# Optimization experiments

Measured on AMD Instinct MI355X. Metric: run time of the kernel, lower is better.

## Reference

```python
import jax, jax.numpy as jnp
import numpy as np
from jax import lax

EPS = 1e-5


def setup_inputs() -> dict:
    key = jax.random.key(0)
    ks = jax.random.split(key, 8)
    b, c_in, h, w = 16, 256, 64, 64
    c_out, kh, n_exp = 512, 3, 8
    fan_in = c_in * kh * kh
    bound_w = float(np.sqrt(6.0 / fan_in))  # kaiming_uniform a=sqrt(5) -> U(-sqrt(6/fan_in), +)
    bound_b = float(1.0 / np.sqrt(fan_in))
    return {
        "x": jax.random.normal(ks[0], (b, c_in, h, w), dtype=jnp.float32),
        "expert_weight": jax.random.uniform(ks[1], (n_exp, c_out, c_in, kh, kh), jnp.float32, -bound_w, bound_w),
        "expert_bias": jax.random.uniform(ks[2], (n_exp, c_out), jnp.float32, -bound_b, bound_b),
        "fc_w": jax.random.uniform(ks[3], (n_exp, c_in), jnp.float32, -1.0 / np.sqrt(c_in), 1.0 / np.sqrt(c_in)),
        "fc_b": jax.random.uniform(ks[4], (n_exp,), jnp.float32, -1.0 / np.sqrt(c_in), 1.0 / np.sqrt(c_in)),
        "bn_gamma": jnp.ones((c_out,), jnp.float32),
        "bn_beta": jnp.zeros((c_out,), jnp.float32),
    }


def reference(x, expert_weight, expert_bias, fc_w, fc_b, bn_gamma, bn_beta):
    # --- route_func: GAP -> Linear -> sigmoid -> (b, k) ---
    pooled = x.mean(axis=(2, 3))                       # (b, c_in)
    routing = jax.nn.sigmoid(pooled @ fc_w.T + fc_b)   # (b, k)

    # --- per-sample combined kernels and biases ---
    comb_w = jnp.einsum('bk,koihw->boihw', routing, expert_weight)  # (b, c_out, c_in, kh, kw)
    comb_b = routing @ expert_bias                                  # (b, c_out)

    # --- per-sample conv (equivalent of groups=b grouped conv) ---
    def conv_one(xi, wi):
        # xi: (c_in, h, w), wi: (c_out, c_in, kh, kw)
        return lax.conv_general_dilated(
            xi[None], wi, window_strides=(1, 1), padding=[(1, 1), (1, 1)],
            rhs_dilation=(1, 1), dimension_numbers=('NCHW', 'OIHW', 'NCHW'))[0]

    out = jax.vmap(conv_one)(x, comb_w) + comb_b[:, :, None, None]  # (b, c_out, h, w)

    # --- BatchNorm2d (training mode: batch statistics) ---
    mean = out.mean(axis=(0, 2, 3))
    var = out.var(axis=(0, 2, 3))
    out = (out - mean[None, :, None, None]) * (bn_gamma * lax.rsqrt(var + EPS))[None, :, None, None] \
          + bn_beta[None, :, None, None]

    # --- LeakyReLU(0.1) ---
    return jnp.where(out > 0, out, 0.1 * out)
```

## Files before the change

kernel.cpp:

```cpp
#include <hip/hip_runtime.h>
#include <hip/hip_bf16.h>
#include <stdint.h>

typedef unsigned short u16;
typedef short bf16x8 __attribute__((ext_vector_type(8)));
typedef float f32x4 __attribute__((ext_vector_type(4)));
typedef u16 u16x8 __attribute__((ext_vector_type(8)));

#define DEVFN static __device__ __forceinline__

#define NB 16
#define CIN 256
#define HH 64
#define WW 64
#define COUT 512
#define NPX 4096
#define NSTEP 72

DEVFN u16 bf16_rne(float f){
  union { float f; uint32_t u; } v; v.f = f;
  uint32_t u = v.u;
  return (u16)((u + 0x7fffu + ((u >> 16) & 1u)) >> 16);
}

DEVFN void gload16(const void* g, void* l){
  __builtin_amdgcn_global_load_lds((const __attribute__((address_space(1))) void*)g,
                                   (__attribute__((address_space(3))) void*)l,
                                   16, 0, 0);
}

#define VMWAIT(N) asm volatile("s_waitcnt vmcnt(" #N ")" ::: "memory")
#define LGKM0() do { asm volatile("s_waitcnt lgkmcnt(0)" ::: "memory"); \
                     __builtin_amdgcn_sched_barrier(0); } while(0)
#define BARRIER() do { __builtin_amdgcn_s_barrier(); \
                       __builtin_amdgcn_sched_barrier(0); \
                       asm volatile("" ::: "memory"); } while(0)

__global__ void k_route(const float* __restrict__ pooled, const float* __restrict__ fcw,
                        const float* __restrict__ fcb, float* __restrict__ routing){
  int bk = blockIdx.x;
  int b = bk >> 3, k = bk & 7;
  int l = threadIdx.x;
  float4 pv = ((const float4*)(pooled + b*CIN))[l];
  float4 wv = ((const float4*)(fcw   + k*CIN))[l];
  float s = pv.x*wv.x + pv.y*wv.y + pv.z*wv.z + pv.w*wv.w;
  for (int o = 32; o; o >>= 1) s += __shfl_down(s, o);
  if (l == 0) routing[b*8 + k] = 1.0f / (1.0f + __expf(-(s * (1.0f/(float)NPX) + fcb[k])));
}

__global__ void k_cbias(const float* __restrict__ routing, const float* __restrict__ eb,
                        float* __restrict__ cbias){
  int idx = blockIdx.x*256 + threadIdx.x;
  int b = idx >> 9, co = idx & 511;
  float s = 0.f;
  for (int k = 0; k < 8; k++) s += routing[b*8+k] * eb[k*COUT + co];
  cbias[idx] = s;
}

__global__ void k_wcomb(const float* __restrict__ routing, const float* __restrict__ ew,
                        u16* __restrict__ wc){
  int blk  = blockIdx.x;
  int step = blk >> 6;
  int cog  = blk & 63;
  int cb = step / 9, rs = step - cb*9;
  int t = threadIdx.x;
  int ci = t & 31, co = cog*8 + (t >> 5);
  int cig = cb*32 + ci;
  float wv[8];
#pragma unroll
  for (int k = 0; k < 8; k++)
    wv[k] = ew[(size_t)((k*COUT + co)*CIN + cig)*9 + rs];
  for (int b = 0; b < NB; b++){
    float s = 0.f;
#pragma unroll
    for (int k = 0; k < 8; k++) s += routing[b*8+k] * wv[k];
    wc[((size_t)(b*NSTEP + step)*COUT + co)*32 + ci] = bf16_rne(s);
  }
}

__global__ void k_halo(u16* __restrict__ xt){
  int blk = blockIdx.x;
  int b = blk / 66, row = blk - b*66;
  uint32_t* base = (uint32_t*)(xt + ((size_t)(b*66 + row))*68*256);
  int t = threadIdx.x;
  if (row == 0 || row == 65){
    for (int i = t; i < 8704; i += 256) base[i] = 0;
  } else {
    for (int i = t; i < 512; i += 256){
      int idx = (i < 128) ? i : (8320 + (i - 128));
      base[idx] = 0;
    }
  }
}

__global__ void k_xprep(const float* __restrict__ x, u16* __restrict__ xt,
                        float* __restrict__ pooled){
  int blk = blockIdx.x;
  int ctile = blk & 3;
  int h = (blk >> 2) & 63;
  int b = blk >> 8;
  __shared__ u16 S[64][66];
  int t = threadIdx.x;
  {
    int ci_l = t >> 2, w0 = (t & 3) * 16;
    const float4* src = (const float4*)(x + ((size_t)((b*CIN + ctile*64 + ci_l)*HH + h)*WW + w0));
    float4 a = src[0], bb = src[1], c = src[2], d = src[3];
    u16* row = &S[ci_l][w0];
    row[0]=bf16_rne(a.x);  row[1]=bf16_rne(a.y);  row[2]=bf16_rne(a.z);  row[3]=bf16_rne(a.w);
    row[4]=bf16_rne(bb.x); row[5]=bf16_rne(bb.y); row[6]=bf16_rne(bb.z); row[7]=bf16_rne(bb.w);
    row[8]=bf16_rne(c.x);  row[9]=bf16_rne(c.y);  row[10]=bf16_rne(c.z); row[11]=bf16_rne(c.w);
    row[12]=bf16_rne(d.x); row[13]=bf16_rne(d.y); row[14]=bf16_rne(d.z); row[15]=bf16_rne(d.w);
    float s = a.x+a.y+a.z+a.w + bb.x+bb.y+bb.z+bb.w + c.x+c.y+c.z+c.w + d.x+d.y+d.z+d.w;
    s += __shfl_down(s, 2);
    s += __shfl_down(s, 1);
    if ((t & 3) == 0) atomicAdd(&pooled[b*CIN + ctile*64 + ci_l], s);
  }
  __syncthreads();
  {
    int w_l = t >> 2, cig = (t & 3) * 16;
    u16x8 v0, v1;
#pragma unroll
    for (int j = 0; j < 8; j++){ v0[j] = S[cig+j][w_l]; v1[j] = S[cig+8+j][w_l]; }
    u16* dst = xt + ((size_t)(b*66 + h + 1)*68 + (w_l + 1))*CIN + ctile*64 + cig;
    *(u16x8*)(dst)     = v0;
    *(u16x8*)(dst + 8) = v1;
  }
}

#define WBYTES 16384
#define XBYTES 26112

template<int H>
DEVFN void stage_w_half(const u16* __restrict__ wstep, char* dst, int wv, int l){
  int qb = H*512 + wv*64;
  int q  = qb + l;
  int co_l = q >> 2, j = q & 3;
  gload16(wstep + co_l*32 + ((j ^ ((co_l >> 1) & 3)) << 3), dst + qb*16);
  __builtin_amdgcn_sched_barrier(0);
}

template<int C>
DEVFN void stage_x_chunk(const u16* __restrict__ xtb, int h0, int cioff, char* dst,
                         int wv, int l){
  int qb = C*512 + wv*64;
  if (qb >= 1632) qb -= 1632;
  int q = qb + l;
  int t2 = q >> 2;
  int lr = (t2 * 964) >> 16;
  int c  = t2 - lr*68;
  int j  = q & 3;
  gload16(xtb + ((size_t)(h0 + lr)*68 + c)*CIN + cioff + ((j ^ ((c >> 1) & 3)) << 3),
          dst + qb*16);
  __builtin_amdgcn_sched_barrier(0);
}

template<int RS>
DEVFN void conv_step(int cb, char* ldsW, const char* Xc, char* Xn,
                     const u16* __restrict__ xtb, const u16* __restrict__ wcb, int h0,
                     int wv, int l, int wm, int wn, int l15, int kbq,
                     f32x4 acc[4][8])
{
  constexpr int r = RS/3, s = RS - r*3;
  const char* Wc = ldsW + (RS % 3)*WBYTES;
  char* Wp       = ldsW + ((RS + 2) % 3)*WBYTES;
  const u16* wnext = wcb + (size_t)(cb*9 + RS + 2)*(COUT*32);
  const bool dostage = (RS <= 6) || (cb < 7);

  bf16x8 wf[4], xf[4];
  const int swzA = (kbq ^ ((l15 >> 1) & 3)) << 4;
#pragma unroll
  for (int nf = 0; nf < 4; nf++)
    wf[nf] = *(const bf16x8*)(Wc + (wn*64 + nf*16 + l15)*64 + swzA);
  {
    int row = wm*2 + r;
#pragma unroll
    for (int mf = 0; mf < 4; mf++){
      int c0 = mf*16 + l15 + s;
      xf[mf] = *(const bf16x8*)(Xc + (row*68 + c0)*64 + ((kbq ^ ((c0 >> 1) & 3)) << 4));
    }
  }
  if (dostage) stage_w_half<0>(wnext, Wp, wv, l);
  BARRIER();
  LGKM0();
  __builtin_amdgcn_s_setprio(1);
#pragma unroll
  for (int nf = 0; nf < 4; nf++)
#pragma unroll
    for (int mf = 0; mf < 4; mf++)
      acc[nf][mf] = __builtin_amdgcn_mfma_f32_16x16x32_bf16(wf[nf], xf[mf], acc[nf][mf], 0, 0, 0);
  __builtin_amdgcn_s_setprio(0);
  BARRIER();

  {
    int row = wm*2 + 1 + r;
#pragma unroll
    for (int mf = 0; mf < 4; mf++){
      int c0 = mf*16 + l15 + s;
      xf[mf] = *(const bf16x8*)(Xc + (row*68 + c0)*64 + ((kbq ^ ((c0 >> 1) & 3)) << 4));
    }
  }
  if (dostage) stage_w_half<1>(wnext, Wp, wv, l);
  if constexpr (RS <= 3) { if (cb < 7) stage_x_chunk<RS>(xtb, h0, (cb+1)*32, Xn, wv, l); }
  if (dostage) { VMWAIT(2); }
  else if constexpr (RS == 7) { VMWAIT(0); }
  BARRIER();
  LGKM0();
  __builtin_amdgcn_s_setprio(1);
#pragma unroll
  for (int nf = 0; nf < 4; nf++)
#pragma unroll
    for (int mf = 0; mf < 4; mf++)
      acc[nf][mf+4] = __builtin_amdgcn_mfma_f32_16x16x32_bf16(wf[nf], xf[mf], acc[nf][mf+4], 0, 0, 0);
  __builtin_amdgcn_s_setprio(0);
  BARRIER();
}

__global__ __launch_bounds__(512, 2) void k_conv(
    const u16* __restrict__ xt, const u16* __restrict__ wc,
    const float* __restrict__ cbias, float* __restrict__ out, u16* __restrict__ obf,
    float* __restrict__ ssum, float* __restrict__ ssq)
{
  __shared__ char lds[3*WBYTES + 2*XBYTES];
  char* XA = lds + 3*WBYTES;
  char* XB = lds + 3*WBYTES + XBYTES;

  int hw  = blockIdx.x;
  int xcd = hw & 7;
  int i   = hw >> 3;
  int b   = xcd*2 + (i >> 5);
  int ct  = (i >> 4) & 1;
  int pt  = i & 15;
  int h0  = pt * 4;

  int t = threadIdx.x, l = t & 63, wv = t >> 6;
  int wm = wv >> 2, wn = wv & 3;
  int l15 = l & 15, kbq = l >> 4;

  const u16* xtb = xt + (size_t)b * 66*68*CIN;
  const u16* wcb = wc + (size_t)(b*NSTEP) * COUT*32 + ct*256*32;

  f32x4 acc[4][8];
#pragma unroll
  for (int nf = 0; nf < 4; nf++)
#pragma unroll
    for (int mf = 0; mf < 8; mf++) acc[nf][mf] = (f32x4){0.f,0.f,0.f,0.f};

  stage_x_chunk<0>(xtb, h0, 0, XA, wv, l);
  stage_x_chunk<1>(xtb, h0, 0, XA, wv, l);
  stage_x_chunk<2>(xtb, h0, 0, XA, wv, l);
  stage_x_chunk<3>(xtb, h0, 0, XA, wv, l);
  stage_w_half<0>(wcb,           lds + 0*WBYTES, wv, l);
  stage_w_half<1>(wcb,           lds + 0*WBYTES, wv, l);
  stage_w_half<0>(wcb + COUT*32, lds + 1*WBYTES, wv, l);
  stage_w_half<1>(wcb + COUT*32, lds + 1*WBYTES, wv, l);
  VMWAIT(0);
  BARRIER();

  for (int cb = 0; cb < 8; cb++){
    const char* Xc = (cb & 1) ? XB : XA;
    char*       Xn = (cb & 1) ? XA : XB;
    conv_step<0>(cb, lds, Xc, Xn, xtb, wcb, h0, wv,l,wm,wn,l15,kbq, acc);
    conv_step<1>(cb, lds, Xc, Xn, xtb, wcb, h0, wv,l,wm,wn,l15,kbq, acc);
    conv_step<2>(cb, lds, Xc, Xn, xtb, wcb, h0, wv,l,wm,wn,l15,kbq, acc);
    conv_step<3>(cb, lds, Xc, Xn, xtb, wcb, h0, wv,l,wm,wn,l15,kbq, acc);
    conv_step<4>(cb, lds, Xc, Xn, xtb, wcb, h0, wv,l,wm,wn,l15,kbq, acc);
    conv_step<5>(cb, lds, Xc, Xn, xtb, wcb, h0, wv,l,wm,wn,l15,kbq, acc);
    conv_step<6>(cb, lds, Xc, Xn, xtb, wcb, h0, wv,l,wm,wn,l15,kbq, acc);
    conv_step<7>(cb, lds, Xc, Xn, xtb, wcb, h0, wv,l,wm,wn,l15,kbq, acc);
    conv_step<8>(cb, lds, Xc, Xn, xtb, wcb, h0, wv,l,wm,wn,l15,kbq, acc);
  }

#pragma unroll
  for (int nf = 0; nf < 4; nf++){
#pragma unroll
    for (int rg = 0; rg < 4; rg++){
      int co = ct*256 + wn*64 + nf*16 + (kbq << 2) + rg;
      float bias = cbias[b*COUT + co];
      float s1 = 0.f, s2 = 0.f;
      size_t base = ((size_t)b * COUT + co) * NPX;
#pragma unroll
      for (int mf = 0; mf < 8; mf++){
        float v = acc[nf][mf][rg] + bias;
        int px = (h0 + wm*2 + (mf >> 2))*64 + (mf & 3)*16 + l15;
        if (obf) obf[base + px] = bf16_rne(v);
        else     out[base + px] = v;
        s1 += v; s2 += v*v;
      }
#pragma unroll
      for (int o = 8; o; o >>= 1){ s1 += __shfl_xor(s1, o); s2 += __shfl_xor(s2, o); }
      if (l15 == 0){ atomicAdd(&ssum[co], s1); atomicAdd(&ssq[co], s2); }
    }
  }
}

__global__ void k_stats(const float* __restrict__ ssum, const float* __restrict__ ssq,
                        const float* __restrict__ gamma, const float* __restrict__ beta,
                        float* __restrict__ sc, float* __restrict__ sh){
  int co = blockIdx.x*256 + threadIdx.x;
  const float invN = 1.0f / 65536.0f;
  float m  = ssum[co] * invN;
  float var = ssq[co] * invN - m*m;
  float scale = gamma[co] * rsqrtf(var + 1e-5f);
  sc[co] = scale;
  sh[co] = beta[co] - m*scale;
}

__global__ void k_norm(float* __restrict__ out, const float* __restrict__ sc,
                       const float* __restrict__ sh){
  const int NF4 = (NB*COUT*NPX)/4;
  int idx = blockIdx.x*256 + threadIdx.x;
  float4* o4 = (float4*)out;
  for (int i = idx; i < NF4; i += 2048*256){
    float4 v = o4[i];
    int co = (i >> 10) & 511;
    float a = sc[co], d = sh[co];
    v.x = fmaf(v.x, a, d); v.y = fmaf(v.y, a, d);
    v.z = fmaf(v.z, a, d); v.w = fmaf(v.w, a, d);
    v.x = v.x > 0.f ? v.x : 0.1f*v.x;
    v.y = v.y > 0.f ? v.y : 0.1f*v.y;
    v.z = v.z > 0.f ? v.z : 0.1f*v.z;
    v.w = v.w > 0.f ? v.w : 0.1f*v.w;
    o4[i] = v;
  }
}

__global__ void k_norm_bf16(const u16* __restrict__ obf, float* __restrict__ out,
                            const float* __restrict__ sc, const float* __restrict__ sh){
  const int NG = (NB*COUT*NPX)/8;
  int idx = blockIdx.x*256 + threadIdx.x;
  for (int g = idx; g < NG; g += 2048*256){
    u16x8 v = *(const u16x8*)(obf + (size_t)g*8);
    int co = (g >> 9) & 511;
    float a = sc[co], d = sh[co];
    float vv[8];
#pragma unroll
    for (int j = 0; j < 8; j++){
      union{ uint32_t u; float f; } c; c.u = ((uint32_t)(u16)v[j]) << 16;
      float w = fmaf(c.f, a, d);
      vv[j] = w > 0.f ? w : 0.1f*w;
    }
    float4* o4 = (float4*)(out + (size_t)g*8);
    o4[0] = (float4){vv[0],vv[1],vv[2],vv[3]};
    o4[1] = (float4){vv[4],vv[5],vv[6],vv[7]};
  }
}

extern "C" void kernel_launch(void* const* d_in, const int* in_sizes, int n_in,
                              void* d_out, int out_size, void* d_ws, size_t ws_size,
                              hipStream_t stream) {
  const float* x     = (const float*)d_in[0];
  const float* ew    = (const float*)d_in[1];
  const float* eb    = (const float*)d_in[2];
  const float* fcw   = (const float*)d_in[3];
  const float* fcb   = (const float*)d_in[4];
  const float* gamma = (const float*)d_in[5];
  const float* beta  = (const float*)d_in[6];
  float* out = (float*)d_out;

  char* ws = (char*)d_ws;
  const size_t XT_BYTES  = (size_t)NB*66*68*CIN*2;
  const size_t WC_BYTES  = (size_t)NB*NSTEP*COUT*32*2;
  const size_t FL_BYTES  = 65536;
  const size_t OBF_BYTES = (size_t)NB*COUT*NPX*2;
  u16* xt = (u16*)ws;
  u16* wc = (u16*)(ws + XT_BYTES);
  float* fbase   = (float*)(ws + XT_BYTES + WC_BYTES);
  float* pooled  = fbase;
  float* ssum    = fbase + 4096;
  float* ssq     = fbase + 4608;
  float* routing = fbase + 5120;
  float* cbias   = fbase + 5248;
  float* sc      = fbase + 13440;
  float* sh      = fbase + 13952;
  bool use_bf16 = ws_size >= XT_BYTES + WC_BYTES + FL_BYTES + OBF_BYTES;
  u16* obf = use_bf16 ? (u16*)(ws + XT_BYTES + WC_BYTES + FL_BYTES) : (u16*)nullptr;

  hipMemsetAsync(pooled, 0, 5120*sizeof(float), stream);

  k_halo <<<1056, 256, 0, stream>>>(xt);
  k_xprep<<<4096, 256, 0, stream>>>(x, xt, pooled);
  k_route<<<128,   64, 0, stream>>>(pooled, fcw, fcb, routing);
  k_cbias<<<32,   256, 0, stream>>>(routing, eb, cbias);
  k_wcomb<<<4608, 256, 0, stream>>>(routing, ew, wc);
  k_conv <<<512,  512, 0, stream>>>(xt, wc, cbias, out, obf, ssum, ssq);
  k_stats<<<2,    256, 0, stream>>>(ssum, ssq, gamma, beta, sc, sh);
  if (use_bf16) k_norm_bf16<<<2048, 256, 0, stream>>>(obf, out, sc, sh);
  else          k_norm     <<<2048, 256, 0, stream>>>(out, sc, sh);
}
```

Before: 273.5 us.

## Halve conv block tile to 2 rows, single-buffer X staged at cb boundary

The conv kernel now runs 1024 blocks of 256 threads (4 waves), each computing 2 output rows instead of 4, with a single X buffer instead of a double-buffered one. The next input-channel chunk of X is loaded during the second half of the final tap step, in a new boundary step, and the last chunk gets a barrier-free tail step. LDS per block shrinks, so more blocks fit per CU, but the weight tile is now reused across half as many pixels, which doubles weight traffic. The X reload also sits on the critical path at each chunk boundary, adding a stall there.

```diff
diff --git a/kernel.cpp b/kernel.cpp
--- a/kernel.cpp
+++ b/kernel.cpp
@@ -128,58 +128,59 @@
 }
 
 #define WBYTES 16384
-#define XBYTES 26112
+#define XBYTES 17408
 
 template<int H>
 DEVFN void stage_w_half(const u16* __restrict__ wstep, char* dst, int wv, int l){
-  int qb = H*512 + wv*64;
-  int q  = qb + l;
-  int co_l = q >> 2, j = q & 3;
-  gload16(wstep + co_l*32 + ((j ^ ((co_l >> 1) & 3)) << 3), dst + qb*16);
+#pragma unroll
+  for (int i = 0; i < 2; i++){
+    int qb = H*512 + i*256 + wv*64;
+    int q  = qb + l;
+    int co_l = q >> 2, j = q & 3;
+    gload16(wstep + co_l*32 + ((j ^ ((co_l >> 1) & 3)) << 3), dst + qb*16);
+  }
   __builtin_amdgcn_sched_barrier(0);
 }
 
-template<int C>
-DEVFN void stage_x_chunk(const u16* __restrict__ xtb, int h0, int cioff, char* dst,
-                         int wv, int l){
-  int qb = C*512 + wv*64;
-  if (qb >= 1632) qb -= 1632;
-  int q = qb + l;
-  int t2 = q >> 2;
-  int lr = (t2 * 964) >> 16;
-  int c  = t2 - lr*68;
-  int j  = q & 3;
-  gload16(xtb + ((size_t)(h0 + lr)*68 + c)*CIN + cioff + ((j ^ ((c >> 1) & 3)) << 3),
-          dst + qb*16);
+DEVFN void stage_x(const u16* __restrict__ xtb, int h0, int cioff, char* dst, int wv, int l){
+#pragma unroll
+  for (int i = 0; i < 5; i++){
+    int qb = i*256 + wv*64;
+    if (qb >= 1088) qb -= 1088;
+    int q = qb + l;
+    int t2 = q >> 2;
+    int lr = (t2 * 964) >> 16;
+    int c  = t2 - lr*68;
+    int j  = q & 3;
+    gload16(xtb + ((size_t)(h0 + lr)*68 + c)*CIN + cioff + ((j ^ ((c >> 1) & 3)) << 3),
+            dst + qb*16);
+  }
   __builtin_amdgcn_sched_barrier(0);
 }
 
 template<int RS>
-DEVFN void conv_step(int cb, char* ldsW, const char* Xc, char* Xn,
-                     const u16* __restrict__ xtb, const u16* __restrict__ wcb, int h0,
-                     int wv, int l, int wm, int wn, int l15, int kbq,
+DEVFN void conv_step(int cb, char* ldsW, const char* Xb,
+                     const u16* __restrict__ wcb,
+                     int wv, int l, int wn, int l15, int kbq,
                      f32x4 acc[4][8])
 {
-  constexpr int r = RS/3, s = RS - r*3;
+  constexpr int r = RS/3, s = RS - (RS/3)*3;
   const char* Wc = ldsW + (RS % 3)*WBYTES;
   char* Wp       = ldsW + ((RS + 2) % 3)*WBYTES;
   const u16* wnext = wcb + (size_t)(cb*9 + RS + 2)*(COUT*32);
-  const bool dostage = (RS <= 6) || (cb < 7);
+  const bool dow = (RS <= 6) || (cb < 7);
 
   bf16x8 wf[4], xf[4];
   const int swzA = (kbq ^ ((l15 >> 1) & 3)) << 4;
 #pragma unroll
   for (int nf = 0; nf < 4; nf++)
     wf[nf] = *(const bf16x8*)(Wc + (wn*64 + nf*16 + l15)*64 + swzA);
-  {
-    int row = wm*2 + r;
-#pragma unroll
-    for (int mf = 0; mf < 4; mf++){
-      int c0 = mf*16 + l15 + s;
-      xf[mf] = *(const bf16x8*)(Xc + (row*68 + c0)*64 + ((kbq ^ ((c0 >> 1) & 3)) << 4));
-    }
-  }
-  if (dostage) stage_w_half<0>(wnext, Wp, wv, l);
+#pragma unroll
+  for (int mf = 0; mf < 4; mf++){
+    int c0 = mf*16 + l15 + s;
+    xf[mf] = *(const bf16x8*)(Xb + (r*68 + c0)*64 + ((kbq ^ ((c0 >> 1) & 3)) << 4));
+  }
+  if (dow) stage_w_half<0>(wnext, Wp, wv, l);
   BARRIER();
   LGKM0();
   __builtin_amdgcn_s_setprio(1);
@@ -191,18 +192,13 @@
   __builtin_amdgcn_s_setprio(0);
   BARRIER();
 
-  {
-    int row = wm*2 + 1 + r;
-#pragma unroll
-    for (int mf = 0; mf < 4; mf++){
-      int c0 = mf*16 + l15 + s;
-      xf[mf] = *(const bf16x8*)(Xc + (row*68 + c0)*64 + ((kbq ^ ((c0 >> 1) & 3)) << 4));
-    }
-  }
-  if (dostage) stage_w_half<1>(wnext, Wp, wv, l);
-  if constexpr (RS <= 3) { if (cb < 7) stage_x_chunk<RS>(xtb, h0, (cb+1)*32, Xn, wv, l); }
-  if (dostage) { VMWAIT(2); }
-  else if constexpr (RS == 7) { VMWAIT(0); }
+#pragma unroll
+  for (int mf = 0; mf < 4; mf++){
+    int c0 = mf*16 + l15 + s;
+    xf[mf] = *(const bf16x8*)(Xb + ((r+1)*68 + c0)*64 + ((kbq ^ ((c0 >> 1) & 3)) << 4));
+  }
+  if (dow) stage_w_half<1>(wnext, Wp, wv, l);
+  if (dow) { VMWAIT(4); } else { VMWAIT(0); }
   BARRIER();
   LGKM0();
   __builtin_amdgcn_s_setprio(1);
@@ -215,25 +211,108 @@
   BARRIER();
 }
 
-__global__ __launch_bounds__(512, 2) void k_conv(
+DEVFN void conv_bound(int cb, char* ldsW, char* Xb,
+                      const u16* __restrict__ xtb, const u16* __restrict__ wcb, int h0,
+                      int wv, int l, int wn, int l15, int kbq,
+                      f32x4 acc[4][8])
+{
+  const char* Wc = ldsW + 2*WBYTES;
+  char* Wp       = ldsW + 1*WBYTES;
+  const u16* wnext = wcb + (size_t)(cb*9 + 10)*(COUT*32);
+
+  bf16x8 wf[4], xf[4];
+  const int swzA = (kbq ^ ((l15 >> 1) & 3)) << 4;
+#pragma unroll
+  for (int nf = 0; nf < 4; nf++)
+    wf[nf] = *(const bf16x8*)(Wc + (wn*64 + nf*16 + l15)*64 + swzA);
+#pragma unroll
+  for (int mf = 0; mf < 4; mf++){
+    int c0 = mf*16 + l15 + 2;
+    xf[mf] = *(const bf16x8*)(Xb + (2*68 + c0)*64 + ((kbq ^ ((c0 >> 1) & 3)) << 4));
+  }
+  stage_w_half<0>(wnext, Wp, wv, l);
+  BARRIER();
+  LGKM0();
+  __builtin_amdgcn_s_setprio(1);
+#pragma unroll
+  for (int nf = 0; nf < 4; nf++)
+#pragma unroll
+    for (int mf = 0; mf < 4; mf++)
+      acc[nf][mf] = __builtin_amdgcn_mfma_f32_16x16x32_bf16(wf[nf], xf[mf], acc[nf][mf], 0, 0, 0);
+  __builtin_amdgcn_s_setprio(0);
+  BARRIER();
+
+#pragma unroll
+  for (int mf = 0; mf < 4; mf++){
+    int c0 = mf*16 + l15 + 2;
+    xf[mf] = *(const bf16x8*)(Xb + (3*68 + c0)*64 + ((kbq ^ ((c0 >> 1) & 3)) << 4));
+  }
+  LGKM0();
+  BARRIER();
+  stage_x(xtb, h0, (cb+1)*32, Xb, wv, l);
+  stage_w_half<1>(wnext, Wp, wv, l);
+  __builtin_amdgcn_s_setprio(1);
+#pragma unroll
+  for (int nf = 0; nf < 4; nf++)
+#pragma unroll
+    for (int mf = 0; mf < 4; mf++)
+      acc[nf][mf+4] = __builtin_amdgcn_mfma_f32_16x16x32_bf16(wf[nf], xf[mf], acc[nf][mf+4], 0, 0, 0);
+  __builtin_amdgcn_s_setprio(0);
+  VMWAIT(0);
+  BARRIER();
+}
+
+DEVFN void conv_last(char* ldsW, const char* Xb,
+                     int wn, int l15, int kbq, f32x4 acc[4][8])
+{
+  const char* Wc = ldsW + 2*WBYTES;
+  bf16x8 wf[4], xf[4];
+  const int swzA = (kbq ^ ((l15 >> 1) & 3)) << 4;
+#pragma unroll
+  for (int nf = 0; nf < 4; nf++)
+    wf[nf] = *(const bf16x8*)(Wc + (wn*64 + nf*16 + l15)*64 + swzA);
+#pragma unroll
+  for (int mf = 0; mf < 4; mf++){
+    int c0 = mf*16 + l15 + 2;
+    xf[mf] = *(const bf16x8*)(Xb + (2*68 + c0)*64 + ((kbq ^ ((c0 >> 1) & 3)) << 4));
+  }
+  LGKM0();
+#pragma unroll
+  for (int nf = 0; nf < 4; nf++)
+#pragma unroll
+    for (int mf = 0; mf < 4; mf++)
+      acc[nf][mf] = __builtin_amdgcn_mfma_f32_16x16x32_bf16(wf[nf], xf[mf], acc[nf][mf], 0, 0, 0);
+#pragma unroll
+  for (int mf = 0; mf < 4; mf++){
+    int c0 = mf*16 + l15 + 2;
+    xf[mf] = *(const bf16x8*)(Xb + (3*68 + c0)*64 + ((kbq ^ ((c0 >> 1) & 3)) << 4));
+  }
+  LGKM0();
+#pragma unroll
+  for (int nf = 0; nf < 4; nf++)
+#pragma unroll
+    for (int mf = 0; mf < 4; mf++)
+      acc[nf][mf+4] = __builtin_amdgcn_mfma_f32_16x16x32_bf16(wf[nf], xf[mf], acc[nf][mf+4], 0, 0, 0);
+}
+
+__global__ __launch_bounds__(256, 2) void k_conv(
     const u16* __restrict__ xt, const u16* __restrict__ wc,
     const float* __restrict__ cbias, float* __restrict__ out, u16* __restrict__ obf,
     float* __restrict__ ssum, float* __restrict__ ssq)
 {
-  __shared__ char lds[3*WBYTES + 2*XBYTES];
-  char* XA = lds + 3*WBYTES;
-  char* XB = lds + 3*WBYTES + XBYTES;
+  __shared__ char lds[3*WBYTES + XBYTES];
+  char* Xb = lds + 3*WBYTES;
 
   int hw  = blockIdx.x;
   int xcd = hw & 7;
   int i   = hw >> 3;
-  int b   = xcd*2 + (i >> 5);
-  int ct  = (i >> 4) & 1;
-  int pt  = i & 15;
-  int h0  = pt * 4;
+  int b   = xcd*2 + (i >> 6);
+  int ct  = (i >> 5) & 1;
+  int pt  = i & 31;
+  int h0  = pt * 2;
 
   int t = threadIdx.x, l = t & 63, wv = t >> 6;
-  int wm = wv >> 2, wn = wv & 3;
+  int wn = wv;
   int l15 = l & 15, kbq = l >> 4;
 
   const u16* xtb = xt + (size_t)b * 66*68*CIN;
@@ -245,29 +324,25 @@
 #pragma unroll
     for (int mf = 0; mf < 8; mf++) acc[nf][mf] = (f32x4){0.f,0.f,0.f,0.f};
 
-  stage_x_chunk<0>(xtb, h0, 0, XA, wv, l);
-  stage_x_chunk<1>(xtb, h0, 0, XA, wv, l);
-  stage_x_chunk<2>(xtb, h0, 0, XA, wv, l);
-  stage_x_chunk<3>(xtb, h0, 0, XA, wv, l);
+  stage_x(xtb, h0, 0, Xb, wv, l);
   stage_w_half<0>(wcb,           lds + 0*WBYTES, wv, l);
   stage_w_half<1>(wcb,           lds + 0*WBYTES, wv, l);
   stage_w_half<0>(wcb + COUT*32, lds + 1*WBYTES, wv, l);
   stage_w_half<1>(wcb + COUT*32, lds + 1*WBYTES, wv, l);
-  VMWAIT(0);
+  VMWAIT(4);
   BARRIER();
 
   for (int cb = 0; cb < 8; cb++){
-    const char* Xc = (cb & 1) ? XB : XA;
-    char*       Xn = (cb & 1) ? XA : XB;
-    conv_step<0>(cb, lds, Xc, Xn, xtb, wcb, h0, wv,l,wm,wn,l15,kbq, acc);
-    conv_step<1>(cb, lds, Xc, Xn, xtb, wcb, h0, wv,l,wm,wn,l15,kbq, acc);
-    conv_step<2>(cb, lds, Xc, Xn, xtb, wcb, h0, wv,l,wm,wn,l15,kbq, acc);
-    conv_step<3>(cb, lds, Xc, Xn, xtb, wcb, h0, wv,l,wm,wn,l15,kbq, acc);
-    conv_step<4>(cb, lds, Xc, Xn, xtb, wcb, h0, wv,l,wm,wn,l15,kbq, acc);
-    conv_step<5>(cb, lds, Xc, Xn, xtb, wcb, h0, wv,l,wm,wn,l15,kbq, acc);
-    conv_step<6>(cb, lds, Xc, Xn, xtb, wcb, h0, wv,l,wm,wn,l15,kbq, acc);
-    conv_step<7>(cb, lds, Xc, Xn, xtb, wcb, h0, wv,l,wm,wn,l15,kbq, acc);
-    conv_step<8>(cb, lds, Xc, Xn, xtb, wcb, h0, wv,l,wm,wn,l15,kbq, acc);
+    conv_step<0>(cb, lds, Xb, wcb, wv,l,wn,l15,kbq, acc);
+    conv_step<1>(cb, lds, Xb, wcb, wv,l,wn,l15,kbq, acc);
+    conv_step<2>(cb, lds, Xb, wcb, wv,l,wn,l15,kbq, acc);
+    conv_step<3>(cb, lds, Xb, wcb, wv,l,wn,l15,kbq, acc);
+    conv_step<4>(cb, lds, Xb, wcb, wv,l,wn,l15,kbq, acc);
+    conv_step<5>(cb, lds, Xb, wcb, wv,l,wn,l15,kbq, acc);
+    conv_step<6>(cb, lds, Xb, wcb, wv,l,wn,l15,kbq, acc);
+    conv_step<7>(cb, lds, Xb, wcb, wv,l,wn,l15,kbq, acc);
+    if (cb < 7) conv_bound(cb, lds, Xb, xtb, wcb, h0, wv,l,wn,l15,kbq, acc);
+    else        conv_last(lds, Xb, wn,l15,kbq, acc);
   }
 
 #pragma unroll
@@ -281,7 +356,7 @@
 #pragma unroll
       for (int mf = 0; mf < 8; mf++){
         float v = acc[nf][mf][rg] + bias;
-        int px = (h0 + wm*2 + (mf >> 2))*64 + (mf & 3)*16 + l15;
+        int px = pt*128 + (mf >> 2)*64 + (mf & 3)*16 + l15;
         if (obf) obf[base + px] = bf16_rne(v);
         else     out[base + px] = v;
         s1 += v; s2 += v*v;
@@ -382,7 +457,7 @@
   k_route<<<128,   64, 0, stream>>>(pooled, fcw, fcb, routing);
   k_cbias<<<32,   256, 0, stream>>>(routing, eb, cbias);
   k_wcomb<<<4608, 256, 0, stream>>>(routing, ew, wc);
-  k_conv <<<512,  512, 0, stream>>>(xt, wc, cbias, out, obf, ssum, ssq);
+  k_conv <<<1024, 256, 0, stream>>>(xt, wc, cbias, out, obf, ssum, ssq);
   k_stats<<<2,    256, 0, stream>>>(ssum, ssq, gamma, beta, sc, sh);
   if (use_bf16) k_norm_bf16<<<2048, 256, 0, stream>>>(obf, out, sc, sh);
   else          k_norm     <<<2048, 256, 0, stream>>>(out, sc, sh);
```

Result: slower. 452.9 us (+65.6%).
